# Performance work log

Measured on AMD Instinct MI355X. Metric: run time of the kernel, lower is better.

Reference implementation:

```python
import jax, jax.numpy as jnp
import numpy as np

N, D, E, H, K = 16384, 256, 8, 512, 2


def setup_inputs() -> dict:
    key = jax.random.key(0)
    ks = jax.random.split(key, 5)
    inputs = jax.random.normal(ks[0], (N, D), dtype=jnp.float32)
    Wg = jax.random.normal(ks[1], (D, E), dtype=jnp.float32) * 0.05
    w1 = jax.random.normal(ks[2], (E, D, H), dtype=jnp.float32) * 0.05
    b1 = jnp.zeros((E, H), dtype=jnp.float32)
    w2 = jax.random.normal(ks[3], (E, H, D), dtype=jnp.float32) * 0.05
    b2 = jnp.zeros((E, D), dtype=jnp.float32)
    return {"inputs": inputs, "Wg": Wg, "w1": w1, "b1": b1, "w2": w2, "b2": b2}


def reference(inputs, Wg, w1, b1, w2, b2):
    # gate + top-k routing (softmax over the selected logits only, as in the torch code)
    gate_logits = inputs @ Wg                       # [N, E]
    topw, topi = jax.lax.top_k(gate_logits, K)      # [N, K]
    topw = jax.nn.softmax(topw.astype(jnp.float32), axis=1).astype(inputs.dtype)
    # combine weights scattered back into a dense [N, E] matrix (dispatch/combine)
    combine = jnp.zeros((N, E), dtype=inputs.dtype)
    combine = combine.at[jnp.arange(N)[:, None], topi].add(topw)  # [N, E]
    # expert MLP (Linear -> GELU(exact) -> Linear), computed per expert and
    # combined with the sparse routing weights (pool='sum')
    h = jax.nn.gelu(jnp.einsum('nd,edh->neh', inputs, w1) + b1[None], approximate=False)  # [N,E,H]
    y = jnp.einsum('neh,ehd->ned', h, w2) + b2[None]                                      # [N,E,D]
    return jnp.einsum('ne,ned->nd', combine, y)                                           # [N,D]
```

## Files before the change

kernel.cpp:

```cpp
#include <hip/hip_runtime.h>

#define NTOK 16384
#define DIM 256
#define NEXP 8
#define HID 512
#define CAP 5120
#define CSTRIDE 16
#define HC 32
#define A2S 40

typedef unsigned short ushort_t;
typedef short bf16x8 __attribute__((ext_vector_type(8)));
typedef float f32x4 __attribute__((ext_vector_type(4)));

#define ASG __attribute__((address_space(1)))
#define ASL __attribute__((address_space(3)))

static __device__ __forceinline__ ushort_t f2bf(float f) {
    unsigned int u = __float_as_uint(f);
    unsigned int r = (u + 0x7FFFu + ((u >> 16) & 1u)) >> 16;
    return (ushort_t)r;
}
static __device__ __forceinline__ float bf2f(ushort_t u) {
    unsigned int x = ((unsigned int)u) << 16;
    return __uint_as_float(x);
}
static __device__ __forceinline__ float gelu_fast(float v) {
    float v2 = v * v;
    float u = v * __builtin_fmaf(v2, -0.1029407079f, -2.3022090196f);
    float e = __builtin_amdgcn_exp2f(u);
    return v * __builtin_amdgcn_rcpf(1.0f + e);
}
#define PIN(x) asm volatile("" : "+v"(x))

__global__ void k_transpose(const float* __restrict__ w1, const float* __restrict__ w2,
                            ushort_t* __restrict__ w1t, ushort_t* __restrict__ w2t,
                            int* __restrict__ counts) {
    __shared__ ushort_t tile[64][72];
    if (blockIdx.x == 0 && threadIdx.x < NEXP * CSTRIDE) counts[threadIdx.x] = 0;
    int b = blockIdx.x;
    const float* src; ushort_t* dst; int R, C, e, t;
    if (b < 256) { e = b >> 5; t = b & 31; src = w1; dst = w1t + e * DIM * HID; R = DIM; C = HID; }
    else { b -= 256; e = b >> 5; t = b & 31; src = w2; dst = w2t + e * DIM * HID; R = HID; C = DIM; }
    size_t ebase = (size_t)e * DIM * HID;
    int tilesC = C >> 6;
    int rt = t / tilesC, ct = t % tilesC;
    for (int i = 0; i < 16; i++) {
        int flat = i * 256 + threadIdx.x;
        int lr = flat >> 6, lc = flat & 63;
        tile[lr][lc] = f2bf(src[ebase + (size_t)(rt * 64 + lr) * C + ct * 64 + lc]);
    }
    __syncthreads();
    for (int i = 0; i < 16; i++) {
        int flat = i * 256 + threadIdx.x;
        int lr = flat >> 6, lc = flat & 63;
        dst[(ct * 64 + lr) * R + rt * 64 + lc] = tile[lc][lr];
    }
}

__global__ void k_router(const float* __restrict__ X, const float* __restrict__ Wg,
                         int* counts, int* tok_list, int* inv_idx, float* inv_w,
                         ushort_t* __restrict__ Xb) {
    __shared__ float xs[64][257];
    __shared__ float lg[64][8];
    __shared__ int te0[64], te1[64], lo0[64], lo1[64];
    __shared__ float tw0[64], tw1[64];
    __shared__ int lcnt[NEXP], gbase[NEXP];
    int tid = threadIdx.x;
    int tok0 = blockIdx.x * 64;
    if (tid < NEXP) lcnt[tid] = 0;
    for (int i = 0; i < 8; i++) {
        int flat = i * 256 + tid;
        int r = flat >> 5, c8 = (flat & 31) << 3;
        const float* row = X + (size_t)(tok0 + r) * DIM + c8;
        float4 a = *(const float4*)row;
        float4 b = *(const float4*)(row + 4);
        xs[r][c8 + 0] = a.x; xs[r][c8 + 1] = a.y; xs[r][c8 + 2] = a.z; xs[r][c8 + 3] = a.w;
        xs[r][c8 + 4] = b.x; xs[r][c8 + 5] = b.y; xs[r][c8 + 6] = b.z; xs[r][c8 + 7] = b.w;
    }
    __syncthreads();
    for (int i = 0; i < 8; i++) {
        int flat = i * 256 + tid;
        int r = flat >> 5, c8 = (flat & 31) << 3;
        ushort_t pk[8];
#pragma unroll
        for (int j = 0; j < 8; j++) pk[j] = f2bf(xs[r][c8 + j]);
        *(int4*)(Xb + (size_t)(tok0 + r) * DIM + c8) = *(const int4*)pk;
    }
    int tl = tid & 63, pair = tid >> 6;
    float l0 = 0.f, l1 = 0.f;
    for (int d = 0; d < DIM; d++) {
        float x = xs[tl][d];
        l0 += x * Wg[d * NEXP + 2 * pair];
        l1 += x * Wg[d * NEXP + 2 * pair + 1];
    }
    lg[tl][2 * pair] = l0; lg[tl][2 * pair + 1] = l1;
    __syncthreads();
    if (tid < 64) {
        float best = -1e30f; int bi = 0;
#pragma unroll
        for (int e = 0; e < NEXP; e++) { float v = lg[tid][e]; if (v > best) { best = v; bi = e; } }
        float best2 = -1e30f; int bi2 = 0;
#pragma unroll
        for (int e = 0; e < NEXP; e++) { if (e == bi) continue; float v = lg[tid][e]; if (v > best2) { best2 = v; bi2 = e; } }
        float ed = __expf(best2 - best);
        te0[tid] = bi; te1[tid] = bi2;
        tw0[tid] = 1.0f / (1.0f + ed);
        tw1[tid] = ed / (1.0f + ed);
        lo0[tid] = atomicAdd(&lcnt[bi], 1);
        lo1[tid] = atomicAdd(&lcnt[bi2], 1);
    }
    __syncthreads();
    if (tid < NEXP) gbase[tid] = atomicAdd(&counts[tid * CSTRIDE], lcnt[tid]);
    __syncthreads();
    if (tid < 64) {
        int token = tok0 + tid;
        int e0 = te0[tid], e1 = te1[tid];
        int p0 = gbase[e0] + lo0[tid]; if (p0 >= CAP) p0 = CAP - 1;
        int p1 = gbase[e1] + lo1[tid]; if (p1 >= CAP) p1 = CAP - 1;
        tok_list[e0 * CAP + p0] = token;
        tok_list[e1 * CAP + p1] = token;
        inv_idx[token * 2]     = (e0 << 16) | p0;  inv_w[token * 2]     = tw0[tid];
        inv_idx[token * 2 + 1] = (e1 << 16) | p1;  inv_w[token * 2 + 1] = tw1[tid];
    }
}

__launch_bounds__(256, 2)
__global__ void k_mlp_fused(const ushort_t* __restrict__ Xb,
                            const ushort_t* __restrict__ w1t, const float* __restrict__ b1,
                            const ushort_t* __restrict__ w2t, const float* __restrict__ b2,
                            const int* __restrict__ counts, const int* __restrict__ tok_list,
                            ushort_t* __restrict__ yb) {
    __shared__ ushort_t A1[2][HC * DIM];
    __shared__ ushort_t A2[2][DIM * HC];
    __shared__ ushort_t HB[64 * A2S];
    int b = blockIdx.x;
    int e = b / 80;
    int tile = b % 80;
    int count = counts[e * CSTRIDE];
    if (count > CAP) count = CAP;
    int t0 = tile * 64;
    if (t0 >= count) return;

    int tid = threadIdx.x;
    int w = tid >> 6, l = tid & 63, ln = l & 15, q = l >> 4;

    int arow = t0 + 16 * w + ln;
    int ci = (arow < count) ? arow : (count - 1);
    int atok = tok_list[e * CAP + ci];
    const ushort_t* xrow = Xb + (size_t)atok * DIM;
    bf16x8 xf[8];
#pragma unroll
    for (int ks = 0; ks < 8; ks++)
        xf[ks] = *(const bf16x8*)(xrow + ks * 32 + q * 8);
#pragma unroll
    for (int ks = 0; ks < 8; ks++) PIN(xf[ks]);

    const ushort_t* w1te = w1t + (size_t)e * DIM * HID;
    const ushort_t* w2te = w2t + (size_t)e * DIM * HID;

    f32x4 zf = {0.f, 0.f, 0.f, 0.f};
    f32x4 yacc[16];
#pragma unroll
    for (int i = 0; i < 16; i++) yacc[i] = zf;

#define STAGE(hcs, pb)                                                                   \
    {                                                                                    \
        _Pragma("unroll")                                                                \
        for (int i = 0; i < 4; i++) {                                                    \
            int g = w * 4 + i;                                                           \
            int r1_ = (g << 1) + (l >> 5);                             \
            int cb1_ = ((l & 31) << 4) ^ ((r1_ & 7) << 4);                               \
            const char* s1_ = (const char*)(w1te + (size_t)((hcs) + r1_) * DIM) + cb1_;  \
            __builtin_amdgcn_global_load_lds((ASG const void*)s1_,                       \
                (ASL void*)((char*)&A1[pb][0] + (g << 10)), 16, 0, 0);                   \
            int r2_ = (g << 4) + (l >> 2);                            \
            int cb2_ = ((l & 3) << 4) ^ ((r2_ & 3) << 4);                                \
            const char* s2_ = (const char*)(w2te + (size_t)r2_ * HID + (hcs)) + cb2_;    \
            __builtin_amdgcn_global_load_lds((ASG const void*)s2_,                       \
                (ASL void*)((char*)&A2[pb][0] + (g << 10)), 16, 0, 0);                   \
        }                                                                                \
    }

    STAGE(0, 0);
    __syncthreads();

    for (int ic = 0; ic < 16; ic++) {
        int hc = ic * HC;
        int p = ic & 1;
        if (ic < 15) STAGE(hc + HC, p ^ 1);

        f32x4 hacc[2];
        hacc[0] = zf; hacc[1] = zf;
#pragma unroll
        for (int ks = 0; ks < 8; ks++) {
            bf16x8 xk = xf[ks];
#pragma unroll
            for (int cf = 0; cf < 2; cf++) {
                int row = cf * 16 + ln;
                bf16x8 wfr = *(const bf16x8*)(&A1[p][row * DIM + (((ks * 4 + q) ^ (row & 7)) << 3)]);
                hacc[cf] = __builtin_amdgcn_mfma_f32_16x16x32_bf16(wfr, xk, hacc[cf], 0, 0, 0);
            }
        }
#pragma unroll
        for (int cf = 0; cf < 2; cf++) {
            float4 bv = *(const float4*)(b1 + e * HID + hc + cf * 16 + q * 4);
            ushort4 pk;
            pk.x = f2bf(gelu_fast(hacc[cf][0] + bv.x));
            pk.y = f2bf(gelu_fast(hacc[cf][1] + bv.y));
            pk.z = f2bf(gelu_fast(hacc[cf][2] + bv.z));
            pk.w = f2bf(gelu_fast(hacc[cf][3] + bv.w));
            *(ushort4*)(HB + (16 * w + ln) * A2S + cf * 16 + q * 4) = pk;
        }
        bf16x8 hf = *(const bf16x8*)(HB + (16 * w + ln) * A2S + q * 8);
#pragma unroll
        for (int cf2 = 0; cf2 < 16; cf2++) {
            int row2 = cf2 * 16 + ln;
            bf16x8 wfr2 = *(const bf16x8*)(&A2[p][row2 * HC + ((q ^ (row2 & 3)) << 3)]);
            yacc[cf2] = __builtin_amdgcn_mfma_f32_16x16x32_bf16(wfr2, hf, yacc[cf2], 0, 0, 0);
        }
        __syncthreads();
    }
    size_t yrowbase = ((size_t)e * CAP + arow) * DIM;
#pragma unroll
    for (int cf2 = 0; cf2 < 16; cf2++) {
        float4 bv = *(const float4*)(b2 + e * DIM + cf2 * 16 + q * 4);
        ushort4 pk;
        pk.x = f2bf(yacc[cf2][0] + bv.x);
        pk.y = f2bf(yacc[cf2][1] + bv.y);
        pk.z = f2bf(yacc[cf2][2] + bv.z);
        pk.w = f2bf(yacc[cf2][3] + bv.w);
        *(ushort4*)(yb + yrowbase + cf2 * 16 + q * 4) = pk;
    }
#undef STAGE
}

__global__ void k_combine(const ushort_t* __restrict__ yb, const int* __restrict__ inv_idx,
                          const float* __restrict__ inv_w, float* __restrict__ out) {
    int tid = threadIdx.x;
    int n = blockIdx.x * 8 + (tid >> 5);
    int l32 = tid & 31, c8 = l32 << 3;
    int i0 = inv_idx[2 * n], i1 = inv_idx[2 * n + 1];
    float w0 = inv_w[2 * n], w1 = inv_w[2 * n + 1];
    size_t r0 = (size_t)(i0 >> 16) * CAP + (i0 & 0xFFFF);
    size_t r1 = (size_t)(i1 >> 16) * CAP + (i1 & 0xFFFF);
    int4 v0 = *(const int4*)(yb + r0 * DIM + c8);
    int4 v1 = *(const int4*)(yb + r1 * DIM + c8);
    ushort_t* p0 = (ushort_t*)&v0;
    ushort_t* p1 = (ushort_t*)&v1;
    float4 oa, ob;
    oa.x = w0 * bf2f(p0[0]) + w1 * bf2f(p1[0]);
    oa.y = w0 * bf2f(p0[1]) + w1 * bf2f(p1[1]);
    oa.z = w0 * bf2f(p0[2]) + w1 * bf2f(p1[2]);
    oa.w = w0 * bf2f(p0[3]) + w1 * bf2f(p1[3]);
    ob.x = w0 * bf2f(p0[4]) + w1 * bf2f(p1[4]);
    ob.y = w0 * bf2f(p0[5]) + w1 * bf2f(p1[5]);
    ob.z = w0 * bf2f(p0[6]) + w1 * bf2f(p1[6]);
    ob.w = w0 * bf2f(p0[7]) + w1 * bf2f(p1[7]);
    float4* op = (float4*)(out + (size_t)n * DIM + c8);
    op[0] = oa; op[1] = ob;
}

extern "C" void kernel_launch(void* const* d_in, const int* in_sizes, int n_in,
                              void* d_out, int out_size, void* d_ws, size_t ws_size,
                              hipStream_t stream) {
    const float* X  = (const float*)d_in[0];
    const float* Wg = (const float*)d_in[1];
    const float* w1 = (const float*)d_in[2];
    const float* b1 = (const float*)d_in[3];
    const float* w2 = (const float*)d_in[4];
    const float* b2 = (const float*)d_in[5];

    char* ws = (char*)d_ws;
    size_t off = 0;
    int* counts = (int*)(ws + off);        off = 1024;
    int* tok_list = (int*)(ws + off);      off += (size_t)NEXP * CAP * 4;
    int* inv_idx = (int*)(ws + off);       off += (size_t)NTOK * 2 * 4;
    float* inv_w = (float*)(ws + off);     off += (size_t)NTOK * 2 * 4;
    ushort_t* w1t = (ushort_t*)(ws + off); off += (size_t)NEXP * DIM * HID * 2;
    ushort_t* w2t = (ushort_t*)(ws + off); off += (size_t)NEXP * DIM * HID * 2;
    ushort_t* Xb = (ushort_t*)(ws + off);  off += (size_t)NTOK * DIM * 2;
    ushort_t* yb = (ushort_t*)(ws + off);  off += (size_t)NEXP * CAP * DIM * 2;

    k_transpose<<<512, 256, 0, stream>>>(w1, w2, w1t, w2t, counts);
    k_router<<<256, 256, 0, stream>>>(X, Wg, counts, tok_list, inv_idx, inv_w, Xb);
    k_mlp_fused<<<NEXP * 80, 256, 0, stream>>>(Xb, w1t, b1, w2t, b2, counts, tok_list, yb);
    k_combine<<<2048, 256, 0, stream>>>(yb, inv_idx, inv_w, (float*)d_out);
}
```

Baseline: 163.3 us.

## Double token tile per block in fused MoE MLP to reuse weight fragments

Each wave now processes two 16-token groups, so each LDS weight fragment feeds two MFMAs and weight staging per token is halved. The grid shrinks from 80 to 40 tiles per expert and launch bounds drop to one block per SM to make room for the doubled accumulators. This trades occupancy and parallelism (fewer blocks than CUs, more tail padding) for less weight load traffic.

```diff
diff --git a/kernel.cpp b/kernel.cpp
--- a/kernel.cpp
+++ b/kernel.cpp
@@ -125,7 +125,7 @@
     }
 }
 
-__launch_bounds__(256, 2)
+__launch_bounds__(256, 1)
 __global__ void k_mlp_fused(const ushort_t* __restrict__ Xb,
                             const ushort_t* __restrict__ w1t, const float* __restrict__ b1,
                             const ushort_t* __restrict__ w2t, const float* __restrict__ b2,
@@ -133,36 +133,42 @@
                             ushort_t* __restrict__ yb) {
     __shared__ ushort_t A1[2][HC * DIM];
     __shared__ ushort_t A2[2][DIM * HC];
-    __shared__ ushort_t HB[64 * A2S];
+    __shared__ ushort_t HB[128 * A2S];
     int b = blockIdx.x;
-    int e = b / 80;
-    int tile = b % 80;
+    int e = b / 40;
+    int tile = b % 40;
     int count = counts[e * CSTRIDE];
     if (count > CAP) count = CAP;
-    int t0 = tile * 64;
+    int t0 = tile * 128;
     if (t0 >= count) return;
 
     int tid = threadIdx.x;
     int w = tid >> 6, l = tid & 63, ln = l & 15, q = l >> 4;
 
-    int arow = t0 + 16 * w + ln;
-    int ci = (arow < count) ? arow : (count - 1);
-    int atok = tok_list[e * CAP + ci];
-    const ushort_t* xrow = Xb + (size_t)atok * DIM;
-    bf16x8 xf[8];
-#pragma unroll
-    for (int ks = 0; ks < 8; ks++)
-        xf[ks] = *(const bf16x8*)(xrow + ks * 32 + q * 8);
-#pragma unroll
-    for (int ks = 0; ks < 8; ks++) PIN(xf[ks]);
+    int arow0 = t0 + 32 * w + ln;
+    int arow1 = arow0 + 16;
+    int ci0 = (arow0 < count) ? arow0 : (count - 1);
+    int ci1 = (arow1 < count) ? arow1 : (count - 1);
+    int tk0 = tok_list[e * CAP + ci0];
+    int tk1 = tok_list[e * CAP + ci1];
+    const ushort_t* xr0 = Xb + (size_t)tk0 * DIM;
+    const ushort_t* xr1 = Xb + (size_t)tk1 * DIM;
+    bf16x8 xf0[8], xf1[8];
+#pragma unroll
+    for (int ks = 0; ks < 8; ks++) {
+        xf0[ks] = *(const bf16x8*)(xr0 + ks * 32 + q * 8);
+        xf1[ks] = *(const bf16x8*)(xr1 + ks * 32 + q * 8);
+    }
+#pragma unroll
+    for (int ks = 0; ks < 8; ks++) { PIN(xf0[ks]); PIN(xf1[ks]); }
 
     const ushort_t* w1te = w1t + (size_t)e * DIM * HID;
     const ushort_t* w2te = w2t + (size_t)e * DIM * HID;
 
     f32x4 zf = {0.f, 0.f, 0.f, 0.f};
-    f32x4 yacc[16];
-#pragma unroll
-    for (int i = 0; i < 16; i++) yacc[i] = zf;
+    f32x4 yacc[16][2];
+#pragma unroll
+    for (int i = 0; i < 16; i++) { yacc[i][0] = zf; yacc[i][1] = zf; }
 
 #define STAGE(hcs, pb)                                                                   \
     {                                                                                    \
@@ -190,47 +196,58 @@
         int p = ic & 1;
         if (ic < 15) STAGE(hc + HC, p ^ 1);
 
-        f32x4 hacc[2];
-        hacc[0] = zf; hacc[1] = zf;
+        f32x4 hacc[2][2];
+        hacc[0][0] = zf; hacc[0][1] = zf; hacc[1][0] = zf; hacc[1][1] = zf;
 #pragma unroll
         for (int ks = 0; ks < 8; ks++) {
-            bf16x8 xk = xf[ks];
 #pragma unroll
             for (int cf = 0; cf < 2; cf++) {
                 int row = cf * 16 + ln;
                 bf16x8 wfr = *(const bf16x8*)(&A1[p][row * DIM + (((ks * 4 + q) ^ (row & 7)) << 3)]);
-                hacc[cf] = __builtin_amdgcn_mfma_f32_16x16x32_bf16(wfr, xk, hacc[cf], 0, 0, 0);
+                hacc[cf][0] = __builtin_amdgcn_mfma_f32_16x16x32_bf16(wfr, xf0[ks], hacc[cf][0], 0, 0, 0);
+                hacc[cf][1] = __builtin_amdgcn_mfma_f32_16x16x32_bf16(wfr, xf1[ks], hacc[cf][1], 0, 0, 0);
             }
         }
 #pragma unroll
         for (int cf = 0; cf < 2; cf++) {
             float4 bv = *(const float4*)(b1 + e * HID + hc + cf * 16 + q * 4);
-            ushort4 pk;
-            pk.x = f2bf(gelu_fast(hacc[cf][0] + bv.x));
-            pk.y = f2bf(gelu_fast(hacc[cf][1] + bv.y));
-            pk.z = f2bf(gelu_fast(hacc[cf][2] + bv.z));
-            pk.w = f2bf(gelu_fast(hacc[cf][3] + bv.w));
-            *(ushort4*)(HB + (16 * w + ln) * A2S + cf * 16 + q * 4) = pk;
+#pragma unroll
+            for (int t = 0; t < 2; t++) {
+                ushort4 pk;
+                pk.x = f2bf(gelu_fast(hacc[cf][t][0] + bv.x));
+                pk.y = f2bf(gelu_fast(hacc[cf][t][1] + bv.y));
+                pk.z = f2bf(gelu_fast(hacc[cf][t][2] + bv.z));
+                pk.w = f2bf(gelu_fast(hacc[cf][t][3] + bv.w));
+                *(ushort4*)(HB + (32 * w + 16 * t + ln) * A2S + cf * 16 + q * 4) = pk;
+            }
         }
-        bf16x8 hf = *(const bf16x8*)(HB + (16 * w + ln) * A2S + q * 8);
+        bf16x8 hf0 = *(const bf16x8*)(HB + (32 * w + ln) * A2S + q * 8);
+        bf16x8 hf1 = *(const bf16x8*)(HB + (32 * w + 16 + ln) * A2S + q * 8);
 #pragma unroll
         for (int cf2 = 0; cf2 < 16; cf2++) {
             int row2 = cf2 * 16 + ln;
             bf16x8 wfr2 = *(const bf16x8*)(&A2[p][row2 * HC + ((q ^ (row2 & 3)) << 3)]);
-            yacc[cf2] = __builtin_amdgcn_mfma_f32_16x16x32_bf16(wfr2, hf, yacc[cf2], 0, 0, 0);
+            yacc[cf2][0] = __builtin_amdgcn_mfma_f32_16x16x32_bf16(wfr2, hf0, yacc[cf2][0], 0, 0, 0);
+            yacc[cf2][1] = __builtin_amdgcn_mfma_f32_16x16x32_bf16(wfr2, hf1, yacc[cf2][1], 0, 0, 0);
         }
         __syncthreads();
     }
-    size_t yrowbase = ((size_t)e * CAP + arow) * DIM;
+    size_t yb0 = ((size_t)e * CAP + arow0) * DIM;
+    size_t yb1 = ((size_t)e * CAP + arow1) * DIM;
 #pragma unroll
     for (int cf2 = 0; cf2 < 16; cf2++) {
         float4 bv = *(const float4*)(b2 + e * DIM + cf2 * 16 + q * 4);
-        ushort4 pk;
-        pk.x = f2bf(yacc[cf2][0] + bv.x);
-        pk.y = f2bf(yacc[cf2][1] + bv.y);
-        pk.z = f2bf(yacc[cf2][2] + bv.z);
-        pk.w = f2bf(yacc[cf2][3] + bv.w);
-        *(ushort4*)(yb + yrowbase + cf2 * 16 + q * 4) = pk;
+        ushort4 pk0, pk1;
+        pk0.x = f2bf(yacc[cf2][0][0] + bv.x);
+        pk0.y = f2bf(yacc[cf2][0][1] + bv.y);
+        pk0.z = f2bf(yacc[cf2][0][2] + bv.z);
+        pk0.w = f2bf(yacc[cf2][0][3] + bv.w);
+        pk1.x = f2bf(yacc[cf2][1][0] + bv.x);
+        pk1.y = f2bf(yacc[cf2][1][1] + bv.y);
+        pk1.z = f2bf(yacc[cf2][1][2] + bv.z);
+        pk1.w = f2bf(yacc[cf2][1][3] + bv.w);
+        *(ushort4*)(yb + yb0 + cf2 * 16 + q * 4) = pk0;
+        *(ushort4*)(yb + yb1 + cf2 * 16 + q * 4) = pk1;
     }
 #undef STAGE
 }
@@ -284,6 +301,6 @@
 
     k_transpose<<<512, 256, 0, stream>>>(w1, w2, w1t, w2t, counts);
     k_router<<<256, 256, 0, stream>>>(X, Wg, counts, tok_list, inv_idx, inv_w, Xb);
-    k_mlp_fused<<<NEXP * 80, 256, 0, stream>>>(Xb, w1t, b1, w2t, b2, counts, tok_list, yb);
+    k_mlp_fused<<<NEXP * 40, 256, 0, stream>>>(Xb, w1t, b1, w2t, b2, counts, tok_list, yb);
     k_combine<<<2048, 256, 0, stream>>>(yb, inv_idx, inv_w, (float*)d_out);
 }
```

New measurement: 184.8 us. 13.1% more time.
